# Optimization experiments

Measured on AMD Instinct MI355X. Metric: run time of the kernel, lower is better.

Reference implementation:

```python
import jax, jax.numpy as jnp
import numpy as np

EPS = 1e-6
K_HOPS = 2  # SGConv K


def setup_inputs() -> dict:
    key = jax.random.key(0)
    k1, k2, k3, k4 = jax.random.split(key, 4)
    B, Kk, C, T = 32, 8, 64, 250
    E, H = 4096, 128
    x = jax.random.normal(k1, (B, Kk, C, T), dtype=jnp.float32)
    edge_index = jax.random.randint(k2, (2, E), 0, C, dtype=jnp.int64)
    edge_weights = jax.random.uniform(k3, (E,), dtype=jnp.float32)
    W = jax.random.normal(k4, (H, Kk * T), dtype=jnp.float32) * 0.02
    b = jnp.zeros((H,), dtype=jnp.float32)
    return {"x": x, "edge_index": edge_index, "edge_weights": edge_weights, "W": W, "b": b}


def reference(x, edge_index, edge_weights, W, b):
    B, Kk, C, T = x.shape
    N = C  # nodes
    x = x.reshape(B, N, Kk * T)  # (B, N, F)

    # clamp non-positive edge weights to epsilon (mirrors in-place .data clamp)
    w = jnp.where(edge_weights <= 0, EPS, edge_weights)

    # gcn_norm with self loops (fill value 1.0)
    src, dst = edge_index[0], edge_index[1]
    loop = jnp.arange(N, dtype=edge_index.dtype)
    src = jnp.concatenate([src, loop])
    dst = jnp.concatenate([dst, loop])
    w = jnp.concatenate([w, jnp.ones((N,), w.dtype)])
    deg = jnp.zeros((N,), w.dtype).at[dst].add(w)
    dinv = jnp.where(deg > 0, deg ** -0.5, jnp.zeros_like(deg))
    norm = dinv[src] * w * dinv[dst]  # (E+N,)

    # K hops of gather -> weight -> scatter-add aggregation
    for _ in range(K_HOPS):
        msg = x[:, src, :] * norm[None, :, None]        # (B, E+N, F)
        x = jnp.zeros_like(x).at[:, dst, :].add(msg)    # (B, N, F)

    # final linear: y = x @ W^T + b
    return jnp.einsum('bnf,hf->bnh', x, W) + b
```

## Files before the change

kernel.cpp:

```cpp
#include <hip/hip_runtime.h>
#include <hip/hip_bf16.h>

#define EPSW 1e-6f

typedef __attribute__((ext_vector_type(4))) float floatx4;
typedef __attribute__((ext_vector_type(8))) short shortx8;

__device__ __forceinline__ unsigned short f2bf(float f) {
    unsigned int u = __float_as_uint(f);
    u = (u + 0x7fffu + ((u >> 16) & 1u)) >> 16;
    return (unsigned short)u;
}

__global__ __launch_bounds__(256) void prep(const float* __restrict__ x,
                                            const float* __restrict__ W,
                                            const int* __restrict__ ei,
                                            const float* __restrict__ ew,
                                            unsigned short* __restrict__ xt,
                                            unsigned short* __restrict__ wt,
                                            float* __restrict__ Mt) {
    __shared__ __align__(16) unsigned char smem[64 * 264 * 2];
    const int bid = blockIdx.x;
    const int t   = threadIdx.x;

    if (bid < 256) {
        unsigned short(*tile)[264] = (unsigned short(*)[264])smem;
        const int rb   = (bid >> 3) * 64;
        const int kgb  = (bid & 7) * 32;
        const int kbas = kgb * 8;
#pragma unroll
        for (int i = 0; i < 16; ++i) {
            const int idx = i * 256 + t;
            const int r   = idx >> 6;
            const int kc  = (idx & 63) * 4;
            const int k   = kbas + kc;
            floatx4 v = (floatx4){0.f, 0.f, 0.f, 0.f};
            if (k < 2000)
                v = *(const floatx4*)(x + (size_t)(rb + r) * 2000 + k);
            tile[r][kc + 0] = f2bf(v.x);
            tile[r][kc + 1] = f2bf(v.y);
            tile[r][kc + 2] = f2bf(v.z);
            tile[r][kc + 3] = f2bf(v.w);
        }
        __syncthreads();
#pragma unroll
        for (int i = 0; i < 8; ++i) {
            const int kg_l = i * 4 + (t >> 6);
            const int r    = t & 63;
            const shortx8 g = *(const shortx8*)&tile[r][kg_l * 8];
            *(shortx8*)(xt + ((size_t)(kgb + kg_l) * 2048 + rb + r) * 8) = g;
        }
    } else if (bid < 272) {
#pragma unroll
        for (int i = 0; i < 8; ++i) {
            const int G  = (bid - 256) * 2048 + i * 256 + t;
            const int kg = G >> 7;
            const int h  = G & 127;
            const int k  = kg * 8;
            floatx4 v0 = (floatx4){0.f, 0.f, 0.f, 0.f};
            floatx4 v1 = (floatx4){0.f, 0.f, 0.f, 0.f};
            if (k < 2000) {
                v0 = *(const floatx4*)(W + (size_t)h * 2000 + k);
                v1 = *(const floatx4*)(W + (size_t)h * 2000 + k + 4);
            }
            unsigned short* p = wt + ((size_t)kg * 128 + h) * 8;
            p[0] = f2bf(v0.x); p[1] = f2bf(v0.y); p[2] = f2bf(v0.z); p[3] = f2bf(v0.w);
            p[4] = f2bf(v1.x); p[5] = f2bf(v1.y); p[6] = f2bf(v1.z); p[7] = f2bf(v1.w);
        }
    } else {
        float* A    = (float*)smem;
        float* deg  = (float*)(smem + 16384);
        float* dinv = deg + 64;
        if (t < 64) deg[t] = 1.0f;
        for (int i = t; i < 4096; i += 256) A[i] = 0.0f;
        __syncthreads();
        const int* src = ei;
        const int* dst = ei + 4096;
        for (int e = t; e < 4096; e += 256) {
            float w = ew[e];
            w = (w <= 0.0f) ? EPSW : w;
            atomicAdd(&deg[dst[e]], w);
        }
        __syncthreads();
        if (t < 64) dinv[t] = 1.0f / sqrtf(deg[t]);
        __syncthreads();
        for (int e = t; e < 4096; e += 256) {
            float w = ew[e];
            w = (w <= 0.0f) ? EPSW : w;
            const int s = src[e], d = dst[e];
            atomicAdd(&A[d * 64 + s], dinv[s] * w * dinv[d]);
        }
        if (t < 64) atomicAdd(&A[t * 64 + t], dinv[t] * dinv[t]);
        __syncthreads();
#pragma unroll
        for (int i = 0; i < 16; ++i) {
            const int idx = i * 256 + t;
            const int n = idx >> 6, c = idx & 63;
            float s = 0.0f;
#pragma unroll 8
            for (int k = 0; k < 64; ++k) s += A[n * 64 + k] * A[k * 64 + c];
            Mt[c * 64 + n] = s;
        }
    }
}

__global__ __launch_bounds__(256) void gemm(const unsigned short* __restrict__ xt,
                                            const unsigned short* __restrict__ wt,
                                            float* __restrict__ z) {
    const int t    = threadIdx.x;
    const int wave = t >> 6, lane = t & 63;
    const int m = lane & 15, q = lane >> 4;
    const int rbase = blockIdx.x * 16;
    const int hbase = blockIdx.y * 64 + wave * 16;

    const shortx8* Ag = (const shortx8*)xt;
    const shortx8* Bg = (const shortx8*)wt;
    int ga = q * 2048 + rbase + m;
    int gb = q * 128 + hbase + m;

    floatx4 acc0 = (floatx4){0.f, 0.f, 0.f, 0.f};
    floatx4 acc1 = (floatx4){0.f, 0.f, 0.f, 0.f};
#pragma unroll 4
    for (int kt = 0; kt < 64; kt += 2) {
        const shortx8 a0 = Ag[ga];
        const shortx8 b0 = Bg[gb];
        const shortx8 a1 = Ag[ga + 8192];
        const shortx8 b1 = Bg[gb + 512];
        acc0 = __builtin_amdgcn_mfma_f32_16x16x32_bf16(a0, b0, acc0, 0, 0, 0);
        acc1 = __builtin_amdgcn_mfma_f32_16x16x32_bf16(a1, b1, acc1, 0, 0, 0);
        ga += 16384; gb += 1024;
    }
#pragma unroll
    for (int v = 0; v < 4; ++v)
        z[(size_t)(rbase + q * 4 + v) * 128 + hbase + m] = acc0[v] + acc1[v];
}

__global__ __launch_bounds__(256) void apply_M(const float* __restrict__ z,
                                               const float* __restrict__ Mtg,
                                               const float* __restrict__ bias,
                                               float* __restrict__ y) {
    __shared__ float Ms[4096];
    __shared__ float zs[64][16];
    const int b  = blockIdx.x;
    const int hc = blockIdx.y;
    const int t  = threadIdx.x;
#pragma unroll
    for (int i = 0; i < 16; ++i) Ms[i * 256 + t] = Mtg[i * 256 + t];
#pragma unroll
    for (int i = 0; i < 4; ++i) {
        const int idx = i * 256 + t;
        const int mr = idx >> 4, hh = idx & 15;
        zs[mr][hh] = z[(size_t)(b * 64 + mr) * 128 + hc * 16 + hh];
    }
    __syncthreads();
    const int h  = t & 15;
    const int n0 = (t >> 4) * 4;
    const float bv = bias[hc * 16 + h];
    float s0 = bv, s1 = bv, s2 = bv, s3 = bv;
#pragma unroll
    for (int mm = 0; mm < 64; ++mm) {
        const float zv = zs[mm][h];
        s0 += Ms[mm * 64 + n0 + 0] * zv;
        s1 += Ms[mm * 64 + n0 + 1] * zv;
        s2 += Ms[mm * 64 + n0 + 2] * zv;
        s3 += Ms[mm * 64 + n0 + 3] * zv;
    }
    float* yp = y + (size_t)b * 8192 + (size_t)n0 * 128 + hc * 16 + h;
    yp[0]   = s0;
    yp[128] = s1;
    yp[256] = s2;
    yp[384] = s3;
}

extern "C" void kernel_launch(void* const* d_in, const int* in_sizes, int n_in,
                              void* d_out, int out_size, void* d_ws, size_t ws_size,
                              hipStream_t stream) {
    const float* x    = (const float*)d_in[0];
    const int*   ei   = (const int*)d_in[1];
    const float* ew   = (const float*)d_in[2];
    const float* W    = (const float*)d_in[3];
    const float* bias = (const float*)d_in[4];
    float* y = (float*)d_out;

    float* z  = (float*)d_ws;
    float* Mt = z + 262144;
    unsigned short* xt = (unsigned short*)(Mt + 4096);
    unsigned short* wt = xt + 4194304;

    prep<<<273, 256, 0, stream>>>(x, W, ei, ew, xt, wt, Mt);
    gemm<<<dim3(128, 2), 256, 0, stream>>>(xt, wt, z);
    apply_M<<<dim3(32, 8), 256, 0, stream>>>(z, Mt, bias, y);
}
```

Baseline: 103.4 us.

## Split GEMM K dimension across waves with LDS reduction and more blocks

```diff
diff --git a/kernel.cpp b/kernel.cpp
--- a/kernel.cpp
+++ b/kernel.cpp
@@ -74,20 +74,24 @@
         if (t < 64) deg[t] = 1.0f;
         for (int i = t; i < 4096; i += 256) A[i] = 0.0f;
         __syncthreads();
-        const int* src = ei;
-        const int* dst = ei + 4096;
-        for (int e = t; e < 4096; e += 256) {
+        const int* srcp = ei;
+        const int* dstp = ei + 4096;
+#pragma unroll
+        for (int i = 0; i < 16; ++i) {
+            const int e = i * 256 + t;
             float w = ew[e];
             w = (w <= 0.0f) ? EPSW : w;
-            atomicAdd(&deg[dst[e]], w);
+            atomicAdd(&deg[dstp[e]], w);
         }
         __syncthreads();
         if (t < 64) dinv[t] = 1.0f / sqrtf(deg[t]);
         __syncthreads();
-        for (int e = t; e < 4096; e += 256) {
+#pragma unroll
+        for (int i = 0; i < 16; ++i) {
+            const int e = i * 256 + t;
             float w = ew[e];
             w = (w <= 0.0f) ? EPSW : w;
-            const int s = src[e], d = dst[e];
+            const int s = srcp[e], d = dstp[e];
             atomicAdd(&A[d * 64 + s], dinv[s] * w * dinv[d]);
         }
         if (t < 64) atomicAdd(&A[t * 64 + t], dinv[t] * dinv[t]);
@@ -104,35 +108,63 @@
     }
 }
 
-__global__ __launch_bounds__(256) void gemm(const unsigned short* __restrict__ xt,
-                                            const unsigned short* __restrict__ wt,
-                                            float* __restrict__ z) {
+__global__ __launch_bounds__(512) void gemm_ksplit(
+        const unsigned short* __restrict__ xt,
+        const unsigned short* __restrict__ wt,
+        float* __restrict__ z) {
+    __shared__ float zsp[8][16][17];
     const int t    = threadIdx.x;
     const int wave = t >> 6, lane = t & 63;
     const int m = lane & 15, q = lane >> 4;
-    const int rbase = blockIdx.x * 16;
-    const int hbase = blockIdx.y * 64 + wave * 16;
+    const int bid = blockIdx.x;
+    const int rt  = bid & 127;
+    const int ht  = bid >> 7;
 
     const shortx8* Ag = (const shortx8*)xt;
     const shortx8* Bg = (const shortx8*)wt;
-    int ga = q * 2048 + rbase + m;
-    int gb = q * 128 + hbase + m;
-
-    floatx4 acc0 = (floatx4){0.f, 0.f, 0.f, 0.f};
-    floatx4 acc1 = (floatx4){0.f, 0.f, 0.f, 0.f};
-#pragma unroll 4
-    for (int kt = 0; kt < 64; kt += 2) {
-        const shortx8 a0 = Ag[ga];
-        const shortx8 b0 = Bg[gb];
-        const shortx8 a1 = Ag[ga + 8192];
-        const shortx8 b1 = Bg[gb + 512];
-        acc0 = __builtin_amdgcn_mfma_f32_16x16x32_bf16(a0, b0, acc0, 0, 0, 0);
-        acc1 = __builtin_amdgcn_mfma_f32_16x16x32_bf16(a1, b1, acc1, 0, 0, 0);
-        ga += 16384; gb += 1024;
-    }
-#pragma unroll
-    for (int v = 0; v < 4; ++v)
-        z[(size_t)(rbase + q * 4 + v) * 128 + hbase + m] = acc0[v] + acc1[v];
+    const int ga = (wave * 32 + q) * 2048 + rt * 16 + m;
+    const int gb = (wave * 32 + q) * 128 + ht * 16 + m;
+
+    shortx8 a0 = Ag[ga];
+    shortx8 a1 = Ag[ga + 8192];
+    shortx8 a2 = Ag[ga + 16384];
+    shortx8 a3 = Ag[ga + 24576];
+    shortx8 a4 = Ag[ga + 32768];
+    shortx8 a5 = Ag[ga + 40960];
+    shortx8 a6 = Ag[ga + 49152];
+    shortx8 a7 = Ag[ga + 57344];
+    shortx8 b0 = Bg[gb];
+    shortx8 b1 = Bg[gb + 512];
+    shortx8 b2 = Bg[gb + 1024];
+    shortx8 b3 = Bg[gb + 1536];
+    shortx8 b4 = Bg[gb + 2048];
+    shortx8 b5 = Bg[gb + 2560];
+    shortx8 b6 = Bg[gb + 3072];
+    shortx8 b7 = Bg[gb + 3584];
+
+    floatx4 accA = (floatx4){0.f, 0.f, 0.f, 0.f};
+    floatx4 accB = (floatx4){0.f, 0.f, 0.f, 0.f};
+    accA = __builtin_amdgcn_mfma_f32_16x16x32_bf16(a0, b0, accA, 0, 0, 0);
+    accB = __builtin_amdgcn_mfma_f32_16x16x32_bf16(a1, b1, accB, 0, 0, 0);
+    accA = __builtin_amdgcn_mfma_f32_16x16x32_bf16(a2, b2, accA, 0, 0, 0);
+    accB = __builtin_amdgcn_mfma_f32_16x16x32_bf16(a3, b3, accB, 0, 0, 0);
+    accA = __builtin_amdgcn_mfma_f32_16x16x32_bf16(a4, b4, accA, 0, 0, 0);
+    accB = __builtin_amdgcn_mfma_f32_16x16x32_bf16(a5, b5, accB, 0, 0, 0);
+    accA = __builtin_amdgcn_mfma_f32_16x16x32_bf16(a6, b6, accA, 0, 0, 0);
+    accB = __builtin_amdgcn_mfma_f32_16x16x32_bf16(a7, b7, accB, 0, 0, 0);
+    accA += accB;
+
+#pragma unroll
+    for (int v = 0; v < 4; ++v) zsp[wave][q * 4 + v][m] = accA[v];
+    __syncthreads();
+
+    if (t < 256) {
+        const int r = t >> 4, c = t & 15;
+        float s = 0.0f;
+#pragma unroll
+        for (int w = 0; w < 8; ++w) s += zsp[w][r][c];
+        z[(size_t)(rt * 16 + r) * 128 + ht * 16 + c] = s;
+    }
 }
 
 __global__ __launch_bounds__(256) void apply_M(const float* __restrict__ z,
@@ -188,6 +220,6 @@
     unsigned short* wt = xt + 4194304;
 
     prep<<<273, 256, 0, stream>>>(x, W, ei, ew, xt, wt, Mt);
-    gemm<<<dim3(128, 2), 256, 0, stream>>>(xt, wt, z);
+    gemm_ksplit<<<1024, 512, 0, stream>>>(xt, wt, z);
     apply_M<<<dim3(32, 8), 256, 0, stream>>>(z, Mt, bias, y);
 }
```

New measurement: 99.67 us. -3.7%, faster.

## Restructure GEMM with LDS double-buffered tiles and split-K partial sums

Applied to the files above, without the earlier changes.

```diff
diff --git a/kernel.cpp b/kernel.cpp
--- a/kernel.cpp
+++ b/kernel.cpp
@@ -12,7 +12,13 @@
     return (unsigned short)u;
 }
 
-__global__ __launch_bounds__(256) void prep(const float* __restrict__ x,
+__device__ __forceinline__ void gl_lds16(const void* g, void* l) {
+    __builtin_amdgcn_global_load_lds(
+        (const __attribute__((address_space(1))) unsigned int*)g,
+        (__attribute__((address_space(3))) unsigned int*)l, 16, 0, 0);
+}
+
+__global__ __launch_bounds__(512) void prep(const float* __restrict__ x,
                                             const float* __restrict__ W,
                                             const int* __restrict__ ei,
                                             const float* __restrict__ ew,
@@ -29,8 +35,8 @@
         const int kgb  = (bid & 7) * 32;
         const int kbas = kgb * 8;
 #pragma unroll
-        for (int i = 0; i < 16; ++i) {
-            const int idx = i * 256 + t;
+        for (int i = 0; i < 8; ++i) {
+            const int idx = i * 512 + t;
             const int r   = idx >> 6;
             const int kc  = (idx & 63) * 4;
             const int k   = kbas + kc;
@@ -44,16 +50,16 @@
         }
         __syncthreads();
 #pragma unroll
-        for (int i = 0; i < 8; ++i) {
-            const int kg_l = i * 4 + (t >> 6);
+        for (int i = 0; i < 4; ++i) {
+            const int kg_l = i * 8 + (t >> 6);
             const int r    = t & 63;
             const shortx8 g = *(const shortx8*)&tile[r][kg_l * 8];
             *(shortx8*)(xt + ((size_t)(kgb + kg_l) * 2048 + rb + r) * 8) = g;
         }
     } else if (bid < 272) {
 #pragma unroll
-        for (int i = 0; i < 8; ++i) {
-            const int G  = (bid - 256) * 2048 + i * 256 + t;
+        for (int i = 0; i < 4; ++i) {
+            const int G  = (bid - 256) * 2048 + i * 512 + t;
             const int kg = G >> 7;
             const int h  = G & 127;
             const int k  = kg * 8;
@@ -72,29 +78,33 @@
         float* deg  = (float*)(smem + 16384);
         float* dinv = deg + 64;
         if (t < 64) deg[t] = 1.0f;
-        for (int i = t; i < 4096; i += 256) A[i] = 0.0f;
-        __syncthreads();
-        const int* src = ei;
-        const int* dst = ei + 4096;
-        for (int e = t; e < 4096; e += 256) {
+        for (int i = t; i < 4096; i += 512) A[i] = 0.0f;
+        __syncthreads();
+        const int* srcp = ei;
+        const int* dstp = ei + 4096;
+#pragma unroll
+        for (int i = 0; i < 8; ++i) {
+            const int e = i * 512 + t;
             float w = ew[e];
             w = (w <= 0.0f) ? EPSW : w;
-            atomicAdd(&deg[dst[e]], w);
+            atomicAdd(&deg[dstp[e]], w);
         }
         __syncthreads();
         if (t < 64) dinv[t] = 1.0f / sqrtf(deg[t]);
         __syncthreads();
-        for (int e = t; e < 4096; e += 256) {
+#pragma unroll
+        for (int i = 0; i < 8; ++i) {
+            const int e = i * 512 + t;
             float w = ew[e];
             w = (w <= 0.0f) ? EPSW : w;
-            const int s = src[e], d = dst[e];
+            const int s = srcp[e], d = dstp[e];
             atomicAdd(&A[d * 64 + s], dinv[s] * w * dinv[d]);
         }
         if (t < 64) atomicAdd(&A[t * 64 + t], dinv[t] * dinv[t]);
         __syncthreads();
 #pragma unroll
-        for (int i = 0; i < 16; ++i) {
-            const int idx = i * 256 + t;
+        for (int i = 0; i < 8; ++i) {
+            const int idx = i * 512 + t;
             const int n = idx >> 6, c = idx & 63;
             float s = 0.0f;
 #pragma unroll 8
@@ -104,38 +114,83 @@
     }
 }
 
-__global__ __launch_bounds__(256) void gemm(const unsigned short* __restrict__ xt,
-                                            const unsigned short* __restrict__ wt,
-                                            float* __restrict__ z) {
+__global__ __launch_bounds__(256) void gemm_lds(
+        const unsigned short* __restrict__ xt,
+        const unsigned short* __restrict__ wt,
+        float* __restrict__ zp) {
+    __shared__ __align__(16) unsigned char smem[2][24576];
     const int t    = threadIdx.x;
     const int wave = t >> 6, lane = t & 63;
     const int m = lane & 15, q = lane >> 4;
-    const int rbase = blockIdx.x * 16;
-    const int hbase = blockIdx.y * 64 + wave * 16;
-
-    const shortx8* Ag = (const shortx8*)xt;
-    const shortx8* Bg = (const shortx8*)wt;
-    int ga = q * 2048 + rbase + m;
-    int gb = q * 128 + hbase + m;
-
-    floatx4 acc0 = (floatx4){0.f, 0.f, 0.f, 0.f};
-    floatx4 acc1 = (floatx4){0.f, 0.f, 0.f, 0.f};
-#pragma unroll 4
-    for (int kt = 0; kt < 64; kt += 2) {
-        const shortx8 a0 = Ag[ga];
-        const shortx8 b0 = Bg[gb];
-        const shortx8 a1 = Ag[ga + 8192];
-        const shortx8 b1 = Bg[gb + 512];
-        acc0 = __builtin_amdgcn_mfma_f32_16x16x32_bf16(a0, b0, acc0, 0, 0, 0);
-        acc1 = __builtin_amdgcn_mfma_f32_16x16x32_bf16(a1, b1, acc1, 0, 0, 0);
-        ga += 16384; gb += 1024;
-    }
-#pragma unroll
-    for (int v = 0; v < 4; ++v)
-        z[(size_t)(rbase + q * 4 + v) * 128 + hbase + m] = acc0[v] + acc1[v];
-}
-
-__global__ __launch_bounds__(256) void apply_M(const float* __restrict__ z,
+    const int bid   = blockIdx.x;
+    const int ks    = bid >> 5;
+    const int rbase = (bid & 31) * 64;
+    const int kg0   = ks * 32;
+
+    floatx4 acc[4][2];
+#pragma unroll
+    for (int rt = 0; rt < 4; ++rt)
+#pragma unroll
+        for (int hh = 0; hh < 2; ++hh)
+            acc[rt][hh] = (floatx4){0.f, 0.f, 0.f, 0.f};
+
+#define ISSUE_CHUNK(c)                                                        \
+    {                                                                         \
+        unsigned char* sb = smem[(c) & 1];                                    \
+        const int ckg = kg0 + (c) * 8;                                        \
+        for (int j = wave; j < 24; j += 4) {                                  \
+            if (j < 8) {                                                      \
+                gl_lds16(xt + ((size_t)(ckg + j) * 2048 + rbase + lane) * 8,  \
+                         sb + j * 1024);                                      \
+            } else {                                                          \
+                const int kgl = (j - 8) >> 1, hf = (j - 8) & 1;               \
+                gl_lds16(wt + ((size_t)(ckg + kgl) * 128 + hf * 64 + lane) * 8,\
+                         sb + 8192 + kgl * 2048 + hf * 1024);                 \
+            }                                                                 \
+        }                                                                     \
+    }
+
+    ISSUE_CHUNK(0);
+    for (int c = 0; c < 4; ++c) {
+        __builtin_amdgcn_s_waitcnt(0);
+        __syncthreads();
+        if (c < 3) ISSUE_CHUNK(c + 1);
+        const unsigned char* sb = smem[c & 1];
+#pragma unroll
+        for (int p = 0; p < 2; ++p) {
+            shortx8 a[4];
+#pragma unroll
+            for (int rt = 0; rt < 4; ++rt)
+                a[rt] = *(const shortx8*)(sb + (p * 4 + q) * 1024 + (rt * 16 + m) * 16);
+            shortx8 bb[2];
+#pragma unroll
+            for (int hh = 0; hh < 2; ++hh)
+                bb[hh] = *(const shortx8*)(sb + 8192 + (p * 4 + q) * 2048 +
+                                           ((wave + hh * 4) * 16 + m) * 16);
+#pragma unroll
+            for (int rt = 0; rt < 4; ++rt)
+#pragma unroll
+                for (int hh = 0; hh < 2; ++hh)
+                    acc[rt][hh] = __builtin_amdgcn_mfma_f32_16x16x32_bf16(
+                        a[rt], bb[hh], acc[rt][hh], 0, 0, 0);
+        }
+        __syncthreads();
+    }
+
+#pragma unroll
+    for (int rt = 0; rt < 4; ++rt)
+#pragma unroll
+        for (int hh = 0; hh < 2; ++hh) {
+            const int h = (wave + hh * 4) * 16 + m;
+#pragma unroll
+            for (int v = 0; v < 4; ++v) {
+                const int row = rbase + rt * 16 + q * 4 + v;
+                zp[((size_t)ks * 2048 + row) * 128 + h] = acc[rt][hh][v];
+            }
+        }
+}
+
+__global__ __launch_bounds__(256) void apply_M(const float* __restrict__ zp,
                                                const float* __restrict__ Mtg,
                                                const float* __restrict__ bias,
                                                float* __restrict__ y) {
@@ -150,7 +205,11 @@
     for (int i = 0; i < 4; ++i) {
         const int idx = i * 256 + t;
         const int mr = idx >> 4, hh = idx & 15;
-        zs[mr][hh] = z[(size_t)(b * 64 + mr) * 128 + hc * 16 + hh];
+        float s = 0.0f;
+#pragma unroll
+        for (int ks = 0; ks < 8; ++ks)
+            s += zp[((size_t)ks * 2048 + b * 64 + mr) * 128 + hc * 16 + hh];
+        zs[mr][hh] = s;
     }
     __syncthreads();
     const int h  = t & 15;
@@ -182,12 +241,12 @@
     const float* bias = (const float*)d_in[4];
     float* y = (float*)d_out;
 
-    float* z  = (float*)d_ws;
-    float* Mt = z + 262144;
+    float* zp = (float*)d_ws;
+    float* Mt = zp + 2097152;
     unsigned short* xt = (unsigned short*)(Mt + 4096);
     unsigned short* wt = xt + 4194304;
 
-    prep<<<273, 256, 0, stream>>>(x, W, ei, ew, xt, wt, Mt);
-    gemm<<<dim3(128, 2), 256, 0, stream>>>(xt, wt, z);
-    apply_M<<<dim3(32, 8), 256, 0, stream>>>(z, Mt, bias, y);
-}
+    prep<<<273, 512, 0, stream>>>(x, W, ei, ew, xt, wt, Mt);
+    gemm_lds<<<256, 256, 0, stream>>>(xt, wt, zp);
+    apply_M<<<dim3(32, 8), 256, 0, stream>>>(zp, Mt, bias, y);
+}
```

After: 97.04 us (median of 2 runs). 1.07x faster.
